# Optimization experiments

Hardware: AMD Instinct MI355X
Metric: run time of the kernel (lower is better)

The kernel has to match this reference:

```python
import jax, jax.numpy as jnp
import numpy as np

N_NODES = 50000
N_EDGES = 600000
D_IN = 128
D_OUT = 128


def setup_inputs() -> dict:
    key = jax.random.key(0)
    ks = jax.random.split(key, 10)
    x = jax.random.normal(ks[0], (N_NODES, D_IN), dtype=jnp.float32)
    # glorot init for per-support weights
    scale = jnp.sqrt(6.0 / (D_IN + D_OUT)).astype(jnp.float32)
    W0 = jax.random.uniform(ks[1], (D_IN, D_OUT), dtype=jnp.float32, minval=-scale, maxval=scale)
    W1 = jax.random.uniform(ks[2], (D_IN, D_OUT), dtype=jnp.float32, minval=-scale, maxval=scale)
    b = jnp.zeros((D_OUT,), dtype=jnp.float32)
    rows0 = jax.random.randint(ks[3], (N_EDGES,), 0, N_NODES, dtype=jnp.int32)
    cols0 = jax.random.randint(ks[4], (N_EDGES,), 0, N_NODES, dtype=jnp.int32)
    vals0 = jax.random.uniform(ks[5], (N_EDGES,), dtype=jnp.float32)
    rows1 = jax.random.randint(ks[6], (N_EDGES,), 0, N_NODES, dtype=jnp.int32)
    cols1 = jax.random.randint(ks[7], (N_EDGES,), 0, N_NODES, dtype=jnp.int32)
    vals1 = jax.random.uniform(ks[8], (N_EDGES,), dtype=jnp.float32)
    return {"x": x, "W0": W0, "W1": W1, "b": b,
            "rows0": rows0, "cols0": cols0, "vals0": vals0,
            "rows1": rows1, "cols1": cols1, "vals1": vals1}


def _spmm(rows, cols, vals, dense, num_rows):
    # sparse (COO) x dense: out[r] = sum_e vals[e] * dense[cols[e]] for rows[e]==r
    gathered = vals[:, None] * dense[cols]  # [E, D]
    return jax.ops.segment_sum(gathered, rows, num_segments=num_rows)


def reference(x, W0, W1, b, rows0, cols0, vals0, rows1, cols1, vals1):
    # support 0: A0 @ (x @ W0); support 1: A1 @ (x @ W1); sum, +bias, relu
    pre0 = x @ W0  # [N, D_OUT]
    pre1 = x @ W1
    s0 = _spmm(rows0, cols0, vals0, pre0, N_NODES)
    s1 = _spmm(rows1, cols1, vals1, pre1, N_NODES)
    out = s0 + s1 + b
    return jax.nn.relu(out)
```

## Files before the change

kernel.cpp:

```cpp
#include <hip/hip_runtime.h>

#define N_NODES 50000
#define N_EDGES 600000
#define D 128
#define SB 98
#define NSEG (2 * SB)
#define CAP 8192
#define HISTBLK 2048
#define BINBLK 4096
#define HIST_BLOCKS ((N_EDGES + HISTBLK - 1) / HISTBLK)
#define BIN_BLOCKS ((N_EDGES + BINBLK - 1) / BINBLK)
#define GEMM_BLOCKS ((N_NODES + 63) / 64)
#define GEMM_A 498
#define GEMM_B 71
#define GEMM_B_ROWBASE (GEMM_A * 64)
#define SPMM_BLOCKS 2048
#define SPMM_WAVES (SPMM_BLOCKS * 4)

typedef __attribute__((ext_vector_type(8))) short short8v;
typedef __attribute__((ext_vector_type(4))) float f32x4;

__device__ __forceinline__ unsigned short f2bf(float f) {
  unsigned u = __float_as_uint(f);
  return (unsigned short)((u + 0x7FFFu + ((u >> 16) & 1u)) >> 16);
}

__device__ __forceinline__ void wpack_one(int idx, const float* __restrict__ W0,
                                          const float* __restrict__ W1,
                                          unsigned short* __restrict__ wpack) {
  const int sup = idx >> 11;
  const int ct = (idx >> 8) & 7;
  const int ks = (idx >> 6) & 3;
  const int l = idx & 63;
  const int q = l >> 4;
  const int c = l & 15;
  const float* W = (sup == 0) ? W0 : W1;
  const int d = ct * 16 + c;
  unsigned short v[8];
#pragma unroll
  for (int i = 0; i < 8; ++i) {
    const int k = ks * 32 + q * 8 + i;
    v[i] = f2bf(W[k * D + d]);
  }
  *(uint4*)(wpack + (size_t)idx * 8) = *(uint4*)v;
}

template <int NW>
__device__ __forceinline__ void gemm_body(
    int block_rowbase, const float* __restrict__ x,
    const unsigned short* __restrict__ wpack, unsigned short* __restrict__ preb,
    unsigned short (*sbuf)[136]) {
  const int t = threadIdx.x;
  const int w = t >> 6;
  const int lane = t & 63;
  const int q = lane >> 4;
  const int c = lane & 15;
  const int arow = block_rowbase + w * 16 + c;

  short8v afrag[4];
#pragma unroll
  for (int ks = 0; ks < 4; ++ks) {
    const int k0 = ks * 32 + q * 8;
    float4 u0 = make_float4(0.f, 0.f, 0.f, 0.f);
    float4 u1 = u0;
    if (arow < N_NODES) {
      u0 = *(const float4*)(x + (size_t)arow * D + k0);
      u1 = *(const float4*)(x + (size_t)arow * D + k0 + 4);
    }
    unsigned short a[8];
    a[0] = f2bf(u0.x); a[1] = f2bf(u0.y); a[2] = f2bf(u0.z); a[3] = f2bf(u0.w);
    a[4] = f2bf(u1.x); a[5] = f2bf(u1.y); a[6] = f2bf(u1.z); a[7] = f2bf(u1.w);
    afrag[ks] = *(const short8v*)a;
  }

  const short8v* wp = (const short8v*)wpack;
#pragma unroll
  for (int sup = 0; sup < 2; ++sup) {
    unsigned short* pb = preb + (size_t)sup * N_NODES * D;
#pragma unroll
    for (int ct = 0; ct < 8; ++ct) {
      f32x4 acc = {0.f, 0.f, 0.f, 0.f};
#pragma unroll
      for (int ks = 0; ks < 4; ++ks) {
        const short8v bfrag = wp[((sup * 8 + ct) * 4 + ks) * 64 + lane];
        acc = __builtin_amdgcn_mfma_f32_16x16x32_bf16(afrag[ks], bfrag, acc,
                                                      0, 0, 0);
      }
#pragma unroll
      for (int j = 0; j < 4; ++j)
        sbuf[w * 16 + q * 4 + j][ct * 16 + c] = f2bf(acc[j]);
    }
    __syncthreads();
#pragma unroll
    for (int it = 0; it < 4; ++it) {
      const int idx = t + it * (NW * 64);
      const int row = idx >> 4;
      const int dseg = (idx & 15) * 8;
      const uint4 v = *(const uint4*)&sbuf[row][dseg];
      const int grow = block_rowbase + row;
      if (grow < N_NODES) *(uint4*)(pb + (size_t)grow * D + dseg) = v;
    }
    __syncthreads();
  }
}

__device__ __forceinline__ void sort_body(int sup, int sb, int s, int n,
                                          int2* __restrict__ cv,
                                          int* __restrict__ rs_s,
                                          int* __restrict__ rs_e,
                                          int* cnt, int* base, int* off) {
  const int t = threadIdx.x;
  if (t < 512) {
    cnt[t] = 0;
    off[t] = 0;
  }
  __syncthreads();

  int2 ed[8];
#pragma unroll
  for (int k = 0; k < 8; ++k) {
    const int i = t + k * 1024;
    if (i < n) {
      ed[k] = cv[s + i];
      atomicAdd(&cnt[(ed[k].x >> 16) & 511], 1);
    }
  }
  __syncthreads();

  if (t < 64) {
    int v[8];
    int ssum = 0;
#pragma unroll
    for (int k = 0; k < 8; ++k) {
      v[k] = cnt[t * 8 + k];
      ssum += v[k];
    }
    int run = ssum;
#pragma unroll
    for (int off2 = 1; off2 < 64; off2 <<= 1) {
      const int u = __shfl_up(run, off2);
      if (t >= off2) run += u;
    }
    int excl = run - ssum;
#pragma unroll
    for (int k = 0; k < 8; ++k) {
      base[t * 8 + k] = excl;
      excl += v[k];
    }
  }
  __syncthreads();

  if (t < 512) {
    const int row = sb * 512 + t;
    if (row < N_NODES) {
      rs_s[sup * N_NODES + row] = s + base[t];
      rs_e[sup * N_NODES + row] = s + base[t] + cnt[t];
    }
  }

#pragma unroll
  for (int k = 0; k < 8; ++k) {
    const int i = t + k * 1024;
    if (i < n) {
      const int rl = (ed[k].x >> 16) & 511;
      const int pos = base[rl] + atomicAdd(&off[rl], 1);
      cv[s + pos] = ed[k];
    }
  }
}

struct BinSmem {
  int hist[SB];
  int lstart[SB];
  int lpos[SB];
  int gbase[SB];
  int2 stage[BINBLK];
};

template <bool CAPPED>
__device__ __forceinline__ void bin_body(
    int bx, const int* __restrict__ rows0, const int* __restrict__ cols0,
    const float* __restrict__ vals0, const int* __restrict__ rows1,
    const int* __restrict__ cols1, const float* __restrict__ vals1,
    int* __restrict__ fillc, int2* __restrict__ cv, BinSmem* sm) {
  const int t = threadIdx.x;
  const int sup = (bx >= BIN_BLOCKS) ? 1 : 0;
  const int bb = bx - sup * BIN_BLOCKS;
  const int* rows = sup ? rows1 : rows0;
  const int* cols = sup ? cols1 : cols0;
  const float* vals = sup ? vals1 : vals0;
  const int ebase = bb * BINBLK;
  const int nloc = min(BINBLK, N_EDGES - ebase);

  if (t < SB) sm->hist[t] = 0;
  __syncthreads();

  int myr[16], myc[16];
  float myv[16];
#pragma unroll
  for (int k = 0; k < 16; ++k) {
    const int i = t + k * 256;
    myr[k] = -1;
    if (i < nloc) {
      myr[k] = rows[ebase + i];
      myc[k] = cols[ebase + i];
      myv[k] = vals[ebase + i];
      atomicAdd(&sm->hist[myr[k] >> 9], 1);
    }
  }
  __syncthreads();

  if (t < 64) {
    const int g0 = 2 * t, g1 = 2 * t + 1;
    const int v0 = (g0 < SB) ? sm->hist[g0] : 0;
    const int v1 = (g1 < SB) ? sm->hist[g1] : 0;
    const int ssum = v0 + v1;
    int run = ssum;
#pragma unroll
    for (int off = 1; off < 64; off <<= 1) {
      const int u = __shfl_up(run, off);
      if (t >= off) run += u;
    }
    const int excl = run - ssum;
    if (g0 < SB) {
      sm->lstart[g0] = excl;
      sm->lpos[g0] = excl;
    }
    if (g1 < SB) {
      sm->lstart[g1] = excl + v0;
      sm->lpos[g1] = excl + v0;
    }
  }
  __syncthreads();

#pragma unroll
  for (int k = 0; k < 16; ++k) {
    if (myr[k] >= 0) {
      const int sb = myr[k] >> 9;
      const int p = atomicAdd(&sm->lpos[sb], 1);
      sm->stage[p] = make_int2(myc[k] | ((myr[k] & 511) << 16) | (sb << 25),
                               __float_as_int(myv[k]));
    }
  }
  if (t < SB && sm->hist[t] > 0) {
    const int seg = sup * SB + t;
    const int bump = atomicAdd(&fillc[seg], sm->hist[t]);
    sm->gbase[t] = (CAPPED ? seg * CAP : 0) + bump;
  }
  __syncthreads();

  for (int i = t; i < nloc; i += 256) {
    const int2 ev = sm->stage[i];
    const int sb = ((unsigned)ev.x) >> 25;
    cv[sm->gbase[sb] + (i - sm->lstart[sb])] = ev;
  }
}

__global__ __launch_bounds__(256) void init_kernel(
    const float* __restrict__ W0, const float* __restrict__ W1,
    unsigned short* __restrict__ wpack, int* __restrict__ fillc) {
  const int t = threadIdx.x;
  if (blockIdx.x == 16) {
    if (t < NSEG) fillc[t] = 0;
    return;
  }
  wpack_one(blockIdx.x * 256 + t, W0, W1, wpack);
}

union BinGemmSmem {
  BinSmem bin;
  unsigned short sbuf[64][136];
};

__global__ __launch_bounds__(256) void bingemmA_kernel(
    const int* __restrict__ rows0, const int* __restrict__ cols0,
    const float* __restrict__ vals0, const int* __restrict__ rows1,
    const int* __restrict__ cols1, const float* __restrict__ vals1,
    int* __restrict__ fillc, int2* __restrict__ cv,
    const float* __restrict__ x, const unsigned short* __restrict__ wpack,
    unsigned short* __restrict__ preb) {
  __shared__ BinGemmSmem sm;
  const int bx = blockIdx.x;
  if (bx >= 2 * BIN_BLOCKS) {
    gemm_body<4>((bx - 2 * BIN_BLOCKS) * 64, x, wpack, preb, sm.sbuf);
    return;
  }
  bin_body<true>(bx, rows0, cols0, vals0, rows1, cols1, vals1, fillc, cv,
                 &sm.bin);
}

union SortGemmSmem {
  struct {
    int cnt[512];
    int base[512];
    int off[512];
  } s;
  unsigned short sbuf[256][136];
};

__global__ __launch_bounds__(1024) void sortgemm_kernel(
    int* __restrict__ fillc, int2* __restrict__ cv, int* __restrict__ rs_s,
    int* __restrict__ rs_e, const float* __restrict__ x,
    const unsigned short* __restrict__ wpack,
    unsigned short* __restrict__ preb) {
  __shared__ SortGemmSmem sm;
  const int bx = blockIdx.x;
  if (bx < NSEG) {
    const int sup = bx / SB;
    const int sb = bx - sup * SB;
    sort_body(sup, sb, bx * CAP, fillc[bx], cv, rs_s, rs_e, sm.s.cnt,
              sm.s.base, sm.s.off);
  } else {
    gemm_body<16>(GEMM_B_ROWBASE + (bx - NSEG) * 256, x, wpack, preb, sm.sbuf);
  }
}

__global__ __launch_bounds__(256) void histpack_kernel(
    const int* __restrict__ rows0, const int* __restrict__ rows1,
    int* __restrict__ cnt, const float* __restrict__ W0,
    const float* __restrict__ W1, unsigned short* __restrict__ wpack) {
  const int t = threadIdx.x;
  if (blockIdx.x >= HIST_BLOCKS) {
    wpack_one(((blockIdx.x - HIST_BLOCKS) + 8 * blockIdx.y) * 256 + t, W0, W1,
              wpack);
    return;
  }
  __shared__ int h[SB];
  if (t < SB) h[t] = 0;
  __syncthreads();
  const int sup = blockIdx.y;
  const int* rows = sup ? rows1 : rows0;
  int e = blockIdx.x * HISTBLK + t;
#pragma unroll
  for (int k = 0; k < HISTBLK / 256; ++k, e += 256)
    if (e < N_EDGES) atomicAdd(&h[rows[e] >> 9], 1);
  __syncthreads();
  if (t < SB && h[t] > 0) atomicAdd(&cnt[sup * SB + t], h[t]);
}

__global__ __launch_bounds__(64) void scan196_kernel(
    const int* __restrict__ cnt, int* __restrict__ fillc,
    int* __restrict__ sbstart) {
  const int t = threadIdx.x;
  int v[4];
  int ssum = 0;
#pragma unroll
  for (int k = 0; k < 4; ++k) {
    const int g = t * 4 + k;
    v[k] = (g < NSEG) ? cnt[g] : 0;
    ssum += v[k];
  }
  int run = ssum;
#pragma unroll
  for (int off = 1; off < 64; off <<= 1) {
    const int u = __shfl_up(run, off);
    if (t >= off) run += u;
  }
  int excl = run - ssum;
#pragma unroll
  for (int k = 0; k < 4; ++k) {
    const int g = t * 4 + k;
    if (g < NSEG) {
      fillc[g] = excl;
      sbstart[g] = excl;
    }
    excl += v[k];
  }
  if (t == 63) sbstart[NSEG] = 2 * N_EDGES;
}

__global__ __launch_bounds__(256) void bingemmB_kernel(
    const int* __restrict__ rows0, const int* __restrict__ cols0,
    const float* __restrict__ vals0, const int* __restrict__ rows1,
    const int* __restrict__ cols1, const float* __restrict__ vals1,
    int* __restrict__ fillc, int2* __restrict__ cv,
    const float* __restrict__ x, const unsigned short* __restrict__ wpack,
    unsigned short* __restrict__ preb) {
  __shared__ BinGemmSmem sm;
  const int bx = blockIdx.x;
  if (bx >= 2 * BIN_BLOCKS) {
    gemm_body<4>((bx - 2 * BIN_BLOCKS) * 64, x, wpack, preb, sm.sbuf);
    return;
  }
  bin_body<false>(bx, rows0, cols0, vals0, rows1, cols1, vals1, fillc, cv,
                  &sm.bin);
}

__global__ __launch_bounds__(1024) void sortB_kernel(
    const int* __restrict__ sbstart, int2* __restrict__ cv,
    int* __restrict__ rs_s, int* __restrict__ rs_e) {
  __shared__ int cnt[512];
  __shared__ int base[512];
  __shared__ int off[512];
  const int sb = blockIdx.x;
  const int sup = blockIdx.y;
  const int seg = sup * SB + sb;
  const int s = sbstart[seg];
  const int n = sbstart[seg + 1] - s;
  sort_body(sup, sb, s, n, cv, rs_s, rs_e, cnt, base, off);
}

__global__ __launch_bounds__(256) void spmm_fused_kernel(
    const int* __restrict__ rs_s, const int* __restrict__ rs_e,
    const int2* __restrict__ cv, const unsigned short* __restrict__ preb,
    const float* __restrict__ bias, float* __restrict__ out) {
  const int lane = threadIdx.x & 63;
  const int g = lane >> 4;
  const int dbase = (lane & 15) << 3;
  const int wid = blockIdx.x * 4 + (threadIdx.x >> 6);

  const float4 b0 = *(const float4*)(bias + dbase);
  const float4 b1 = *(const float4*)(bias + dbase + 4);

  for (int row = wid; row < N_NODES; row += SPMM_WAVES) {
    float acc[8];
#pragma unroll
    for (int i = 0; i < 8; ++i) acc[i] = 0.f;

#pragma unroll
    for (int sup = 0; sup < 2; ++sup) {
      const int s = rs_s[sup * N_NODES + row];
      const int e = rs_e[sup * N_NODES + row];
      const unsigned short* pb = preb + (size_t)sup * N_NODES * D;
      int j = s + g;
      for (; j + 4 < e; j += 8) {
        const int2 e0 = cv[j];
        const int2 e1 = cv[j + 4];
        const uint4 q0 = *(const uint4*)(pb + (size_t)(e0.x & 0xFFFF) * D + dbase);
        const uint4 q1 = *(const uint4*)(pb + (size_t)(e1.x & 0xFFFF) * D + dbase);
        const float v0 = __int_as_float(e0.y);
        const float v1 = __int_as_float(e1.y);
        acc[0] = fmaf(v0, __uint_as_float(q0.x << 16), acc[0]);
        acc[1] = fmaf(v0, __uint_as_float(q0.x & 0xFFFF0000u), acc[1]);
        acc[2] = fmaf(v0, __uint_as_float(q0.y << 16), acc[2]);
        acc[3] = fmaf(v0, __uint_as_float(q0.y & 0xFFFF0000u), acc[3]);
        acc[4] = fmaf(v0, __uint_as_float(q0.z << 16), acc[4]);
        acc[5] = fmaf(v0, __uint_as_float(q0.z & 0xFFFF0000u), acc[5]);
        acc[6] = fmaf(v0, __uint_as_float(q0.w << 16), acc[6]);
        acc[7] = fmaf(v0, __uint_as_float(q0.w & 0xFFFF0000u), acc[7]);
        acc[0] = fmaf(v1, __uint_as_float(q1.x << 16), acc[0]);
        acc[1] = fmaf(v1, __uint_as_float(q1.x & 0xFFFF0000u), acc[1]);
        acc[2] = fmaf(v1, __uint_as_float(q1.y << 16), acc[2]);
        acc[3] = fmaf(v1, __uint_as_float(q1.y & 0xFFFF0000u), acc[3]);
        acc[4] = fmaf(v1, __uint_as_float(q1.z << 16), acc[4]);
        acc[5] = fmaf(v1, __uint_as_float(q1.z & 0xFFFF0000u), acc[5]);
        acc[6] = fmaf(v1, __uint_as_float(q1.w << 16), acc[6]);
        acc[7] = fmaf(v1, __uint_as_float(q1.w & 0xFFFF0000u), acc[7]);
      }
      if (j < e) {
        const int2 e0 = cv[j];
        const uint4 q0 = *(const uint4*)(pb + (size_t)(e0.x & 0xFFFF) * D + dbase);
        const float v0 = __int_as_float(e0.y);
        acc[0] = fmaf(v0, __uint_as_float(q0.x << 16), acc[0]);
        acc[1] = fmaf(v0, __uint_as_float(q0.x & 0xFFFF0000u), acc[1]);
        acc[2] = fmaf(v0, __uint_as_float(q0.y << 16), acc[2]);
        acc[3] = fmaf(v0, __uint_as_float(q0.y & 0xFFFF0000u), acc[3]);
        acc[4] = fmaf(v0, __uint_as_float(q0.z << 16), acc[4]);
        acc[5] = fmaf(v0, __uint_as_float(q0.z & 0xFFFF0000u), acc[5]);
        acc[6] = fmaf(v0, __uint_as_float(q0.w << 16), acc[6]);
        acc[7] = fmaf(v0, __uint_as_float(q0.w & 0xFFFF0000u), acc[7]);
      }
    }

#pragma unroll
    for (int i = 0; i < 8; ++i) {
      acc[i] += __shfl_xor(acc[i], 16);
      acc[i] += __shfl_xor(acc[i], 32);
    }

    if (g == 0) {
      float4 r0, r1;
      r0.x = fmaxf(acc[0] + b0.x, 0.f);
      r0.y = fmaxf(acc[1] + b0.y, 0.f);
      r0.z = fmaxf(acc[2] + b0.z, 0.f);
      r0.w = fmaxf(acc[3] + b0.w, 0.f);
      r1.x = fmaxf(acc[4] + b1.x, 0.f);
      r1.y = fmaxf(acc[5] + b1.y, 0.f);
      r1.z = fmaxf(acc[6] + b1.z, 0.f);
      r1.w = fmaxf(acc[7] + b1.w, 0.f);
      float* op = out + (size_t)row * D + dbase;
      *(float4*)op = r0;
      *(float4*)(op + 4) = r1;
    }
  }
}

__global__ __launch_bounds__(256) void gemm_f32_kernel(
    const float* __restrict__ x, const float* __restrict__ W,
    float* __restrict__ pre) {
  const int tid = threadIdx.x;
  const int nloc = (tid >> 5) << 3;
  const int d4 = (tid & 31) << 2;
  const int nbase = blockIdx.x * 64;
  __shared__ float xs[64][D];
  {
    float4* xs4 = (float4*)(&xs[0][0]);
    const float4* xg4 = (const float4*)x;
#pragma unroll
    for (int i = 0; i < 8; ++i) {
      const int idx = tid + i * 256;
      const int row = nbase + (idx >> 5);
      xs4[idx] = (row < N_NODES) ? xg4[(size_t)row * 32 + (idx & 31)]
                                 : make_float4(0.f, 0.f, 0.f, 0.f);
    }
  }
  __syncthreads();
  float4 acc[8];
#pragma unroll
  for (int i = 0; i < 8; ++i) acc[i] = make_float4(0.f, 0.f, 0.f, 0.f);
  for (int k = 0; k < D; ++k) {
    const float4 w = *(const float4*)(W + k * D + d4);
#pragma unroll
    for (int i = 0; i < 8; ++i) {
      const float xv = xs[nloc + i][k];
      acc[i].x = fmaf(xv, w.x, acc[i].x);
      acc[i].y = fmaf(xv, w.y, acc[i].y);
      acc[i].z = fmaf(xv, w.z, acc[i].z);
      acc[i].w = fmaf(xv, w.w, acc[i].w);
    }
  }
#pragma unroll
  for (int i = 0; i < 8; ++i) {
    const int n = nbase + nloc + i;
    if (n < N_NODES) *(float4*)(pre + (size_t)n * D + d4) = acc[i];
  }
}

__global__ __launch_bounds__(256) void spmm_scatter_kernel(
    const int* __restrict__ rows, const int* __restrict__ cols,
    const float* __restrict__ vals, const float* __restrict__ pre,
    float* __restrict__ out) {
  const long long idx = (long long)blockIdx.x * blockDim.x + threadIdx.x;
  const int e = (int)(idx >> 6);
  if (e >= N_EDGES) return;
  const int dd = ((int)idx & 63) << 1;
  const int r = rows[e];
  const int c = cols[e];
  const float v = vals[e];
  const float2 p = *(const float2*)(pre + (size_t)c * D + dd);
  float* outp = out + (size_t)r * D + dd;
  atomicAdd(outp + 0, v * p.x);
  atomicAdd(outp + 1, v * p.y);
}

__global__ __launch_bounds__(256) void bias_relu_kernel(
    float* __restrict__ out, const float* __restrict__ b) {
  const int idx = blockIdx.x * blockDim.x + threadIdx.x;
  float4 v = ((float4*)out)[idx];
  const float4 bb = ((const float4*)b)[idx & 31];
  v.x = fmaxf(v.x + bb.x, 0.f);
  v.y = fmaxf(v.y + bb.y, 0.f);
  v.z = fmaxf(v.z + bb.z, 0.f);
  v.w = fmaxf(v.w + bb.w, 0.f);
  ((float4*)out)[idx] = v;
}

extern "C" void kernel_launch(void* const* d_in, const int* in_sizes, int n_in,
                              void* d_out, int out_size, void* d_ws,
                              size_t ws_size, hipStream_t stream) {
  const float* x = (const float*)d_in[0];
  const float* W0 = (const float*)d_in[1];
  const float* W1 = (const float*)d_in[2];
  const float* b = (const float*)d_in[3];
  const int* rows0 = (const int*)d_in[4];
  const int* cols0 = (const int*)d_in[5];
  const float* vals0 = (const float*)d_in[6];
  const int* rows1 = (const int*)d_in[7];
  const int* cols1 = (const int*)d_in[8];
  const float* vals1 = (const float*)d_in[9];
  float* out = (float*)d_out;

  auto align_up = [](size_t v) { return (v + 255) & ~(size_t)255; };
  const size_t PREB = align_up((size_t)2 * N_NODES * D * 2);
  const size_t FILLC = align_up((size_t)NSEG * 4);
  const size_t RS1 = align_up((size_t)2 * N_NODES * 4);
  const size_t WPACK = align_up((size_t)2 * D * D * 2);

  const size_t CVC = align_up((size_t)NSEG * CAP * 8);
  const size_t NEED_A = PREB + CVC + FILLC + 2 * RS1 + WPACK;
  const size_t CV = align_up((size_t)2 * N_EDGES * 8);
  const size_t CNT = align_up((size_t)NSEG * 4);
  const size_t SBSTART = align_up((size_t)(NSEG + 1) * 4);
  const size_t NEED_B = PREB + CV + CNT + FILLC + SBSTART + 2 * RS1 + WPACK;

  char* wsc = (char*)d_ws;

  if (ws_size >= NEED_A) {
    unsigned short* preb = (unsigned short*)wsc;
    int2* cv = (int2*)(wsc + PREB);
    int* fillc = (int*)(wsc + PREB + CVC);
    int* rs_s = (int*)(wsc + PREB + CVC + FILLC);
    int* rs_e = (int*)(wsc + PREB + CVC + FILLC + RS1);
    unsigned short* wpack =
        (unsigned short*)(wsc + PREB + CVC + FILLC + 2 * RS1);

    init_kernel<<<17, 256, 0, stream>>>(W0, W1, wpack, fillc);
    bingemmA_kernel<<<2 * BIN_BLOCKS + GEMM_A, 256, 0, stream>>>(
        rows0, cols0, vals0, rows1, cols1, vals1, fillc, cv, x, wpack, preb);
    sortgemm_kernel<<<NSEG + GEMM_B, 1024, 0, stream>>>(fillc, cv, rs_s, rs_e,
                                                        x, wpack, preb);
    spmm_fused_kernel<<<SPMM_BLOCKS, 256, 0, stream>>>(rs_s, rs_e, cv, preb, b,
                                                       out);
  } else if (ws_size >= NEED_B) {
    unsigned short* preb = (unsigned short*)wsc;
    int2* cv = (int2*)(wsc + PREB);
    int* cnt = (int*)(wsc + PREB + CV);
    int* fillc = (int*)(wsc + PREB + CV + CNT);
    int* sbstart = (int*)(wsc + PREB + CV + CNT + FILLC);
    int* rs_s = (int*)(wsc + PREB + CV + CNT + FILLC + SBSTART);
    int* rs_e = (int*)(wsc + PREB + CV + CNT + FILLC + SBSTART + RS1);
    unsigned short* wpack =
        (unsigned short*)(wsc + PREB + CV + CNT + FILLC + SBSTART + 2 * RS1);

    hipMemsetAsync(cnt, 0, (size_t)NSEG * 4, stream);
    histpack_kernel<<<dim3(HIST_BLOCKS + 8, 2), 256, 0, stream>>>(
        rows0, rows1, cnt, W0, W1, wpack);
    scan196_kernel<<<1, 64, 0, stream>>>(cnt, fillc, sbstart);
    bingemmB_kernel<<<2 * BIN_BLOCKS + GEMM_BLOCKS, 256, 0, stream>>>(
        rows0, cols0, vals0, rows1, cols1, vals1, fillc, cv, x, wpack, preb);
    sortB_kernel<<<dim3(SB, 2), 1024, 0, stream>>>(sbstart, cv, rs_s, rs_e);
    spmm_fused_kernel<<<SPMM_BLOCKS, 256, 0, stream>>>(rs_s, rs_e, cv, preb, b,
                                                       out);
  } else {
    float* pre = (float*)wsc;
    hipMemsetAsync(d_out, 0, (size_t)N_NODES * D * 4, stream);
    const int scat_blocks = (N_EDGES * 64 + 255) / 256;
    gemm_f32_kernel<<<GEMM_BLOCKS, 256, 0, stream>>>(x, W0, pre);
    spmm_scatter_kernel<<<scat_blocks, 256, 0, stream>>>(rows0, cols0, vals0,
                                                         pre, out);
    gemm_f32_kernel<<<GEMM_BLOCKS, 256, 0, stream>>>(x, W1, pre);
    spmm_scatter_kernel<<<scat_blocks, 256, 0, stream>>>(rows1, cols1, vals1,
                                                         pre, out);
    bias_relu_kernel<<<(N_NODES * D / 4) / 256, 256, 0, stream>>>(out, b);
  }
}
```

Before: 98.86 us.

## Halve row-bucket size to 256 rows and move all GEMM into bin kernel

Changes the row super-bucket from 512 to 256 rows, doubling the segment count to 392 and halving the per-segment capacity. The sort blocks now handle half as many edges each, with more of them running in parallel. The GEMM work that was split between the bin kernel and the sort kernel now runs entirely alongside the bin blocks, leaving a pure sort kernel. The cost is more segments, more global atomics on fill counters, and a denser bit encoding in the packed edge word. With CAP at 4096, the default path also carries a higher risk of a segment overflowing its capacity.

Measured after the change: 88.43 us. 10.5% less time.

```diff
diff --git a/kernel.cpp b/kernel.cpp
--- a/kernel.cpp
+++ b/kernel.cpp
@@ -3,17 +3,16 @@
 #define N_NODES 50000
 #define N_EDGES 600000
 #define D 128
-#define SB 98
+#define SB 196
+#define SBROWS 256
+#define SBSHIFT 8
 #define NSEG (2 * SB)
-#define CAP 8192
+#define CAP 4096
 #define HISTBLK 2048
 #define BINBLK 4096
 #define HIST_BLOCKS ((N_EDGES + HISTBLK - 1) / HISTBLK)
 #define BIN_BLOCKS ((N_EDGES + BINBLK - 1) / BINBLK)
 #define GEMM_BLOCKS ((N_NODES + 63) / 64)
-#define GEMM_A 498
-#define GEMM_B 71
-#define GEMM_B_ROWBASE (GEMM_A * 64)
 #define SPMM_BLOCKS 2048
 #define SPMM_WAVES (SPMM_BLOCKS * 4)
 
@@ -45,8 +44,7 @@
   *(uint4*)(wpack + (size_t)idx * 8) = *(uint4*)v;
 }
 
-template <int NW>
-__device__ __forceinline__ void gemm_body(
+__device__ __forceinline__ void gemm_body64(
     int block_rowbase, const float* __restrict__ x,
     const unsigned short* __restrict__ wpack, unsigned short* __restrict__ preb,
     unsigned short (*sbuf)[136]) {
@@ -93,7 +91,7 @@
     __syncthreads();
 #pragma unroll
     for (int it = 0; it < 4; ++it) {
-      const int idx = t + it * (NW * 64);
+      const int idx = t + it * 256;
       const int row = idx >> 4;
       const int dseg = (idx & 15) * 8;
       const uint4 v = *(const uint4*)&sbuf[row][dseg];
@@ -110,29 +108,29 @@
                                           int* __restrict__ rs_e,
                                           int* cnt, int* base, int* off) {
   const int t = threadIdx.x;
-  if (t < 512) {
+  if (t < SBROWS) {
     cnt[t] = 0;
     off[t] = 0;
   }
   __syncthreads();
 
-  int2 ed[8];
-#pragma unroll
-  for (int k = 0; k < 8; ++k) {
+  int2 ed[4];
+#pragma unroll
+  for (int k = 0; k < 4; ++k) {
     const int i = t + k * 1024;
     if (i < n) {
       ed[k] = cv[s + i];
-      atomicAdd(&cnt[(ed[k].x >> 16) & 511], 1);
+      atomicAdd(&cnt[(ed[k].x >> 16) & (SBROWS - 1)], 1);
     }
   }
   __syncthreads();
 
   if (t < 64) {
-    int v[8];
+    int v[4];
     int ssum = 0;
 #pragma unroll
-    for (int k = 0; k < 8; ++k) {
-      v[k] = cnt[t * 8 + k];
+    for (int k = 0; k < 4; ++k) {
+      v[k] = cnt[t * 4 + k];
       ssum += v[k];
     }
     int run = ssum;
@@ -143,15 +141,15 @@
     }
     int excl = run - ssum;
 #pragma unroll
-    for (int k = 0; k < 8; ++k) {
-      base[t * 8 + k] = excl;
+    for (int k = 0; k < 4; ++k) {
+      base[t * 4 + k] = excl;
       excl += v[k];
     }
   }
   __syncthreads();
 
-  if (t < 512) {
-    const int row = sb * 512 + t;
+  if (t < SBROWS) {
+    const int row = sb * SBROWS + t;
     if (row < N_NODES) {
       rs_s[sup * N_NODES + row] = s + base[t];
       rs_e[sup * N_NODES + row] = s + base[t] + cnt[t];
@@ -159,10 +157,10 @@
   }
 
 #pragma unroll
-  for (int k = 0; k < 8; ++k) {
+  for (int k = 0; k < 4; ++k) {
     const int i = t + k * 1024;
     if (i < n) {
-      const int rl = (ed[k].x >> 16) & 511;
+      const int rl = (ed[k].x >> 16) & (SBROWS - 1);
       const int pos = base[rl] + atomicAdd(&off[rl], 1);
       cv[s + pos] = ed[k];
     }
@@ -205,30 +203,35 @@
       myr[k] = rows[ebase + i];
       myc[k] = cols[ebase + i];
       myv[k] = vals[ebase + i];
-      atomicAdd(&sm->hist[myr[k] >> 9], 1);
+      atomicAdd(&sm->hist[myr[k] >> SBSHIFT], 1);
     }
   }
   __syncthreads();
 
   if (t < 64) {
-    const int g0 = 2 * t, g1 = 2 * t + 1;
-    const int v0 = (g0 < SB) ? sm->hist[g0] : 0;
-    const int v1 = (g1 < SB) ? sm->hist[g1] : 0;
-    const int ssum = v0 + v1;
+    int v[4];
+    int ssum = 0;
+#pragma unroll
+    for (int k = 0; k < 4; ++k) {
+      const int g = t * 4 + k;
+      v[k] = (g < SB) ? sm->hist[g] : 0;
+      ssum += v[k];
+    }
     int run = ssum;
 #pragma unroll
     for (int off = 1; off < 64; off <<= 1) {
       const int u = __shfl_up(run, off);
       if (t >= off) run += u;
     }
-    const int excl = run - ssum;
-    if (g0 < SB) {
-      sm->lstart[g0] = excl;
-      sm->lpos[g0] = excl;
-    }
-    if (g1 < SB) {
-      sm->lstart[g1] = excl + v0;
-      sm->lpos[g1] = excl + v0;
+    int excl = run - ssum;
+#pragma unroll
+    for (int k = 0; k < 4; ++k) {
+      const int g = t * 4 + k;
+      if (g < SB) {
+        sm->lstart[g] = excl;
+        sm->lpos[g] = excl;
+      }
+      excl += v[k];
     }
   }
   __syncthreads();
@@ -236,10 +239,11 @@
 #pragma unroll
   for (int k = 0; k < 16; ++k) {
     if (myr[k] >= 0) {
-      const int sb = myr[k] >> 9;
+      const int sb = myr[k] >> SBSHIFT;
       const int p = atomicAdd(&sm->lpos[sb], 1);
-      sm->stage[p] = make_int2(myc[k] | ((myr[k] & 511) << 16) | (sb << 25),
-                               __float_as_int(myv[k]));
+      sm->stage[p] =
+          make_int2(myc[k] | ((myr[k] & (SBROWS - 1)) << 16) | (sb << 24),
+                    __float_as_int(myv[k]));
     }
   }
   if (t < SB && sm->hist[t] > 0) {
@@ -251,7 +255,7 @@
 
   for (int i = t; i < nloc; i += 256) {
     const int2 ev = sm->stage[i];
-    const int sb = ((unsigned)ev.x) >> 25;
+    const int sb = ((unsigned)ev.x) >> 24;
     cv[sm->gbase[sb] + (i - sm->lstart[sb])] = ev;
   }
 }
@@ -262,6 +266,7 @@
   const int t = threadIdx.x;
   if (blockIdx.x == 16) {
     if (t < NSEG) fillc[t] = 0;
+    if (t + 256 < NSEG) fillc[t + 256] = 0;
     return;
   }
   wpack_one(blockIdx.x * 256 + t, W0, W1, wpack);
@@ -272,7 +277,8 @@
   unsigned short sbuf[64][136];
 };
 
-__global__ __launch_bounds__(256) void bingemmA_kernel(
+template <bool CAPPED>
+__global__ __launch_bounds__(256) void bingemm_kernel(
     const int* __restrict__ rows0, const int* __restrict__ cols0,
     const float* __restrict__ vals0, const int* __restrict__ rows1,
     const int* __restrict__ cols1, const float* __restrict__ vals1,
@@ -282,37 +288,23 @@
   __shared__ BinGemmSmem sm;
   const int bx = blockIdx.x;
   if (bx >= 2 * BIN_BLOCKS) {
-    gemm_body<4>((bx - 2 * BIN_BLOCKS) * 64, x, wpack, preb, sm.sbuf);
+    gemm_body64((bx - 2 * BIN_BLOCKS) * 64, x, wpack, preb, sm.sbuf);
     return;
   }
-  bin_body<true>(bx, rows0, cols0, vals0, rows1, cols1, vals1, fillc, cv,
-                 &sm.bin);
-}
-
-union SortGemmSmem {
-  struct {
-    int cnt[512];
-    int base[512];
-    int off[512];
-  } s;
-  unsigned short sbuf[256][136];
-};
-
-__global__ __launch_bounds__(1024) void sortgemm_kernel(
-    int* __restrict__ fillc, int2* __restrict__ cv, int* __restrict__ rs_s,
-    int* __restrict__ rs_e, const float* __restrict__ x,
-    const unsigned short* __restrict__ wpack,
-    unsigned short* __restrict__ preb) {
-  __shared__ SortGemmSmem sm;
-  const int bx = blockIdx.x;
-  if (bx < NSEG) {
-    const int sup = bx / SB;
-    const int sb = bx - sup * SB;
-    sort_body(sup, sb, bx * CAP, fillc[bx], cv, rs_s, rs_e, sm.s.cnt,
-              sm.s.base, sm.s.off);
-  } else {
-    gemm_body<16>(GEMM_B_ROWBASE + (bx - NSEG) * 256, x, wpack, preb, sm.sbuf);
-  }
+  bin_body<CAPPED>(bx, rows0, cols0, vals0, rows1, cols1, vals1, fillc, cv,
+                   &sm.bin);
+}
+
+__global__ __launch_bounds__(1024) void sortA_kernel(
+    const int* __restrict__ fillc, int2* __restrict__ cv,
+    int* __restrict__ rs_s, int* __restrict__ rs_e) {
+  __shared__ int cnt[SBROWS];
+  __shared__ int base[SBROWS];
+  __shared__ int off[SBROWS];
+  const int sb = blockIdx.x;
+  const int sup = blockIdx.y;
+  const int seg = sup * SB + sb;
+  sort_body(sup, sb, seg * CAP, fillc[seg], cv, rs_s, rs_e, cnt, base, off);
 }
 
 __global__ __launch_bounds__(256) void histpack_kernel(
@@ -333,20 +325,20 @@
   int e = blockIdx.x * HISTBLK + t;
 #pragma unroll
   for (int k = 0; k < HISTBLK / 256; ++k, e += 256)
-    if (e < N_EDGES) atomicAdd(&h[rows[e] >> 9], 1);
+    if (e < N_EDGES) atomicAdd(&h[rows[e] >> SBSHIFT], 1);
   __syncthreads();
   if (t < SB && h[t] > 0) atomicAdd(&cnt[sup * SB + t], h[t]);
 }
 
-__global__ __launch_bounds__(64) void scan196_kernel(
+__global__ __launch_bounds__(64) void scanseg_kernel(
     const int* __restrict__ cnt, int* __restrict__ fillc,
     int* __restrict__ sbstart) {
   const int t = threadIdx.x;
-  int v[4];
+  int v[7];
   int ssum = 0;
 #pragma unroll
-  for (int k = 0; k < 4; ++k) {
-    const int g = t * 4 + k;
+  for (int k = 0; k < 7; ++k) {
+    const int g = t * 7 + k;
     v[k] = (g < NSEG) ? cnt[g] : 0;
     ssum += v[k];
   }
@@ -358,8 +350,8 @@
   }
   int excl = run - ssum;
 #pragma unroll
-  for (int k = 0; k < 4; ++k) {
-    const int g = t * 4 + k;
+  for (int k = 0; k < 7; ++k) {
+    const int g = t * 7 + k;
     if (g < NSEG) {
       fillc[g] = excl;
       sbstart[g] = excl;
@@ -369,29 +361,12 @@
   if (t == 63) sbstart[NSEG] = 2 * N_EDGES;
 }
 
-__global__ __launch_bounds__(256) void bingemmB_kernel(
-    const int* __restrict__ rows0, const int* __restrict__ cols0,
-    const float* __restrict__ vals0, const int* __restrict__ rows1,
-    const int* __restrict__ cols1, const float* __restrict__ vals1,
-    int* __restrict__ fillc, int2* __restrict__ cv,
-    const float* __restrict__ x, const unsigned short* __restrict__ wpack,
-    unsigned short* __restrict__ preb) {
-  __shared__ BinGemmSmem sm;
-  const int bx = blockIdx.x;
-  if (bx >= 2 * BIN_BLOCKS) {
-    gemm_body<4>((bx - 2 * BIN_BLOCKS) * 64, x, wpack, preb, sm.sbuf);
-    return;
-  }
-  bin_body<false>(bx, rows0, cols0, vals0, rows1, cols1, vals1, fillc, cv,
-                  &sm.bin);
-}
-
 __global__ __launch_bounds__(1024) void sortB_kernel(
     const int* __restrict__ sbstart, int2* __restrict__ cv,
     int* __restrict__ rs_s, int* __restrict__ rs_e) {
-  __shared__ int cnt[512];
-  __shared__ int base[512];
-  __shared__ int off[512];
+  __shared__ int cnt[SBROWS];
+  __shared__ int base[SBROWS];
+  __shared__ int off[SBROWS];
   const int sb = blockIdx.x;
   const int sup = blockIdx.y;
   const int seg = sup * SB + sb;
@@ -595,10 +570,9 @@
         (unsigned short*)(wsc + PREB + CVC + FILLC + 2 * RS1);
 
     init_kernel<<<17, 256, 0, stream>>>(W0, W1, wpack, fillc);
-    bingemmA_kernel<<<2 * BIN_BLOCKS + GEMM_A, 256, 0, stream>>>(
+    bingemm_kernel<true><<<2 * BIN_BLOCKS + GEMM_BLOCKS, 256, 0, stream>>>(
         rows0, cols0, vals0, rows1, cols1, vals1, fillc, cv, x, wpack, preb);
-    sortgemm_kernel<<<NSEG + GEMM_B, 1024, 0, stream>>>(fillc, cv, rs_s, rs_e,
-                                                        x, wpack, preb);
+    sortA_kernel<<<dim3(SB, 2), 1024, 0, stream>>>(fillc, cv, rs_s, rs_e);
     spmm_fused_kernel<<<SPMM_BLOCKS, 256, 0, stream>>>(rs_s, rs_e, cv, preb, b,
                                                        out);
   } else if (ws_size >= NEED_B) {
@@ -615,8 +589,8 @@
     hipMemsetAsync(cnt, 0, (size_t)NSEG * 4, stream);
     histpack_kernel<<<dim3(HIST_BLOCKS + 8, 2), 256, 0, stream>>>(
         rows0, rows1, cnt, W0, W1, wpack);
-    scan196_kernel<<<1, 64, 0, stream>>>(cnt, fillc, sbstart);
-    bingemmB_kernel<<<2 * BIN_BLOCKS + GEMM_BLOCKS, 256, 0, stream>>>(
+    scanseg_kernel<<<1, 64, 0, stream>>>(cnt, fillc, sbstart);
+    bingemm_kernel<false><<<2 * BIN_BLOCKS + GEMM_BLOCKS, 256, 0, stream>>>(
         rows0, cols0, vals0, rows1, cols1, vals1, fillc, cv, x, wpack, preb);
     sortB_kernel<<<dim3(SB, 2), 1024, 0, stream>>>(sbstart, cv, rs_s, rs_e);
     spmm_fused_kernel<<<SPMM_BLOCKS, 256, 0, stream>>>(rs_s, rs_e, cv, preb, b,
```
